# Kernel optimization log

Measured on AMD Instinct MI355X. Metric: run time of the kernel, lower is better.

## Reference

```python
import jax, jax.numpy as jnp
import numpy as np

GRID_SIZE = 5
SPLINE_ORDER = 3
GRID_MIN = -1.0
GRID_MAX = 1.0
H = (GRID_MAX - GRID_MIN) / GRID_SIZE          # grid interval
G0 = GRID_MIN - SPLINE_ORDER * H               # first (extended) knot = grid[:,0]


def _basis_matrix():
    # Uniform B-spline power-basis matrix, same recurrence as the torch code.
    M = np.array([[1.0]], dtype=np.float64)
    scalar = 1.0
    for k in range(2, SPLINE_ORDER + 2):
        t1 = np.pad(M, ((0, 1), (0, 0)))
        t3 = np.pad(M, ((1, 0), (0, 0)))
        t2 = np.zeros((k - 1, k))
        t4 = np.zeros((k - 1, k))
        for i in range(k - 1):
            t2[i, i] = i + 1
            t2[i, i + 1] = k - (i + 2)
            t4[i, i] = -1.0
            t4[i, i + 1] = 1.0
        M = t1 @ t2 + t3 @ t4
        scalar *= 1.0 / (k - 1)
    return (M * scalar).astype(np.float32)

BASIS = jnp.asarray(_basis_matrix())  # (spline_order+1, spline_order+1)


def setup_inputs():
    key = jax.random.key(0)
    k1, k2, k3 = jax.random.split(key, 3)
    N, FIN, FOUT = 2048, 128, 128
    x = jax.random.normal(k1, (N, FIN), dtype=jnp.float32)
    base_weight = jax.random.normal(k2, (FOUT, FIN), dtype=jnp.float32) * 0.1
    spline_weight = jax.random.normal(k3, (FIN, FOUT, GRID_SIZE + SPLINE_ORDER), dtype=jnp.float32) * 0.1
    return {"x": x, "base_weight": base_weight, "spline_weight": spline_weight}


def _forward(x, base_weight, spline_weight):
    N, fin = x.shape
    fout = base_weight.shape[0]
    k = SPLINE_ORDER
    # base branch: SiLU activation then linear
    base_out = jax.nn.silu(x) @ base_weight.T                       # (N, fout)
    # input normalization: Hardtanh around grid center (shift=0, scale=1 for [-1,1])
    shift = (GRID_MIN + GRID_MAX) / 2.0
    scale = (GRID_MAX - GRID_MIN) / 2.0
    xn = jnp.clip((x - shift) / scale, -1.0, 1.0) * scale + shift
    # bucketize: bin index + fractional position (replaces floor/compare + torch.nonzero)
    t = (xn - G0) / H
    fl = jnp.floor(t)
    u1 = t - fl                                                     # (x - interval_floor) / interval
    idx = jnp.clip(fl.astype(jnp.int32), k, k + GRID_SIZE - 1)      # clamped knot-interval index
    cfloor = idx - k                                                # (N, fin) first control point index
    # power bases [1, u, u^2, ..., u^k] -> b-spline basis via basis matrix
    pows = u1[..., None] ** jnp.arange(k + 1, dtype=x.dtype)        # (N, fin, k+1)
    bspl = pows @ BASIS.astype(x.dtype)                             # (N, fin, k+1)
    # faithful to torch: spline_weight.view(out, in, -1) memory reinterpretation
    cp = jnp.reshape(spline_weight, (fout, fin, GRID_SIZE + k))
    gidx = cfloor[..., None] + jnp.arange(k + 1)                    # (N, fin, k+1) control point indices
    i_idx = jnp.arange(fin)[None, :, None]
    gathered = cp[:, i_idx, gidx]                                   # (fout, N, fin, k+1)
    gathered = jnp.transpose(gathered, (1, 0, 2, 3))                # (N, fout, fin, k+1)
    # faithful to torch: .view(N, in, k+1, out) memory reinterpretation
    cpr = jnp.reshape(gathered, (N, fin, k + 1, fout))
    # per-feature spline matmul then sum over in_features (KAN aggregation)
    spline_out = jnp.einsum('nij,nijo->no', bspl, cpr)              # (N, fout)
    return base_out + spline_out


def reference(x, base_weight, spline_weight):
    return _forward(x, base_weight, spline_weight)
```

## Files before the change

kernel.cpp:

```cpp
#include <hip/hip_runtime.h>
#include <hip/hip_bf16.h>
#include <math.h>

typedef __attribute__((ext_vector_type(8))) short short8;
typedef __attribute__((ext_vector_type(4))) float floatx4;
typedef float v4fu __attribute__((ext_vector_type(4), aligned(4)));

#define WS_S    0u
#define WS_P    524288u
#define WS_BT   2621440u
#define WS_C    2916352u
#define WS_T    3178496u

__global__ __launch_bounds__(256) void kan_prep(
    const float* __restrict__ x, const float* __restrict__ bw,
    const float* __restrict__ sw, unsigned char* __restrict__ ws)
{
    __hip_bfloat16* S  = (__hip_bfloat16*)(ws + WS_S);
    __hip_bfloat16* P  = (__hip_bfloat16*)(ws + WS_P);
    __hip_bfloat16* Bt = (__hip_bfloat16*)(ws + WS_BT);
    unsigned char*  cb = ws + WS_C;
    int g = blockIdx.x * 256 + threadIdx.x;
    if (g < 262144) {
        float xv = x[g];
        float si = xv / (1.0f + expf(-xv));
        float xn = fminf(fmaxf(xv, -1.0f), 1.0f);
        float t  = (xn + 2.2f) / 0.4f;
        float u  = t - floorf(t);
        int idx  = (int)floorf(t);
        idx = min(max(idx, 3), 7);
        cb[g] = (unsigned char)(idx - 3);
        float u2 = u*u, u3 = u2*u, om = 1.0f - u;
        float b0 = om*om*om*(1.0f/6.0f);
        float b1 = 0.5f*u3 - u2 + (2.0f/3.0f);
        float b2 = -0.5f*u3 + 0.5f*u2 + 0.5f*u + (1.0f/6.0f);
        float b3 = u3*(1.0f/6.0f);
        S[g] = __float2bfloat16(si);
        P[0*262144 + g] = __float2bfloat16(b0);
        P[1*262144 + g] = __float2bfloat16(b1);
        P[2*262144 + g] = __float2bfloat16(b2);
        P[3*262144 + g] = __float2bfloat16(b3);
    } else if (g < 262144 + 131072) {
        int g2 = g - 262144;
        int a = g2 >> 10, j = g2 & 1023;
        Bt[j*128 + a] = __float2bfloat16(sw[g2]);
    } else if (g < 262144 + 131072 + 16384) {
        int g3 = g - 393216;
        Bt[131072 + g3] = __float2bfloat16(bw[g3]);
    }
}

__global__ __launch_bounds__(256) void kan_gemm(unsigned char* __restrict__ ws)
{
    __shared__ __align__(16) __hip_bfloat16 sA[32 * 128];
    __shared__ __align__(16) __hip_bfloat16 sB[64 * 128];
    const int tid = threadIdx.x;
    const int n0  = blockIdx.x * 32;
    const int j0  = blockIdx.y * 64;
    const __hip_bfloat16* Ap = (const __hip_bfloat16*)(ws + ((j0 >= 1024) ? WS_S : (WS_P + (unsigned)(j0 >> 8) * 524288u)));
    const __hip_bfloat16* Bp = (const __hip_bfloat16*)(ws + WS_BT);

#pragma unroll
    for (int i = 0; i < 2; ++i) {
        int c = tid + 256*i, r = c >> 4, k8 = c & 15;
        *(uint4*)(sA + r*128 + k8*8) = *(const uint4*)(Ap + (n0 + r)*128 + k8*8);
    }
#pragma unroll
    for (int i = 0; i < 4; ++i) {
        int c = tid + 256*i, r = c >> 4, k8 = c & 15;
        *(uint4*)(sB + r*128 + k8*8) = *(const uint4*)(Bp + (j0 + r)*128 + k8*8);
    }
    __syncthreads();

    const int w = tid >> 6, l = tid & 63;
    const int mt = w & 1, nth = w >> 1;
    const int m = l & 15, q = l >> 4;
    floatx4 acc0 = {0.f,0.f,0.f,0.f}, acc1 = {0.f,0.f,0.f,0.f};
    const int arow  = (mt*16      + m)*128 + q*8;
    const int brow0 = (nth*32     + m)*128 + q*8;
    const int brow1 = (nth*32 + 16 + m)*128 + q*8;
#pragma unroll
    for (int kk = 0; kk < 4; ++kk) {
        short8 a  = *(const short8*)(sA + arow  + kk*32);
        short8 b0 = *(const short8*)(sB + brow0 + kk*32);
        short8 b1 = *(const short8*)(sB + brow1 + kk*32);
        acc0 = __builtin_amdgcn_mfma_f32_16x16x32_bf16(a, b0, acc0, 0, 0, 0);
        acc1 = __builtin_amdgcn_mfma_f32_16x16x32_bf16(a, b1, acc1, 0, 0, 0);
    }
    float* T = (float*)(ws + WS_T);
    const int row  = n0 + mt*16 + q*4;
    const int col0 = j0 + nth*32 + m;
#pragma unroll
    for (int r = 0; r < 4; ++r) {
        T[(row + r)*1152 + col0]      = acc0[r];
        T[(row + r)*1152 + col0 + 16] = acc1[r];
    }
}

__global__ __launch_bounds__(256) void kan_epi(const unsigned char* __restrict__ ws,
                                               float* __restrict__ out)
{
    int g = blockIdx.x * 256 + threadIdx.x;
    int n = g >> 5, oh = g & 31;
    const unsigned char* cb = ws + WS_C + n*128;
    const float* Tr = (const float*)(ws + WS_T) + n*1152;
    v4fu acc = *(const v4fu*)(Tr + 1024 + 4*oh);
#pragma unroll
    for (int b = 0; b < 4; ++b) {
        int c = cb[32*b + oh];
        acc += *(const v4fu*)(Tr + 256*b + 8*oh + c);
    }
    *(v4fu*)(out + n*128 + 4*oh) = acc;
}

extern "C" void kernel_launch(void* const* d_in, const int* in_sizes, int n_in,
                              void* d_out, int out_size, void* d_ws, size_t ws_size,
                              hipStream_t stream) {
    const float* x  = (const float*)d_in[0];
    const float* bw = (const float*)d_in[1];
    const float* sw = (const float*)d_in[2];
    float* out = (float*)d_out;
    unsigned char* ws = (unsigned char*)d_ws;
    kan_prep<<<dim3(1600), dim3(256), 0, stream>>>(x, bw, sw, ws);
    kan_gemm<<<dim3(64, 18), dim3(256), 0, stream>>>(ws);
    kan_epi <<<dim3(256), dim3(256), 0, stream>>>(ws, out);
}
```

Measured before the change: 70.70 us.

## Fuse basis computation, GEMM and gather epilogue into one split-K kernel with atomics

Result: slower. 96.22 us (+36.1%).

```diff
diff --git a/kernel.cpp b/kernel.cpp
--- a/kernel.cpp
+++ b/kernel.cpp
@@ -4,113 +4,207 @@
 
 typedef __attribute__((ext_vector_type(8))) short short8;
 typedef __attribute__((ext_vector_type(4))) float floatx4;
-typedef float v4fu __attribute__((ext_vector_type(4), aligned(4)));
-
-#define WS_S    0u
-#define WS_P    524288u
-#define WS_BT   2621440u
-#define WS_C    2916352u
-#define WS_T    3178496u
+
+static __device__ __forceinline__ unsigned short bfbits(float f) {
+    __hip_bfloat16 h = __float2bfloat16(f);
+    unsigned short u;
+    __builtin_memcpy(&u, &h, 2);
+    return u;
+}
+static __device__ __forceinline__ unsigned pack2(float lo, float hi) {
+    return (unsigned)bfbits(lo) | ((unsigned)bfbits(hi) << 16);
+}
 
 __global__ __launch_bounds__(256) void kan_prep(
-    const float* __restrict__ x, const float* __restrict__ bw,
-    const float* __restrict__ sw, unsigned char* __restrict__ ws)
+    const float* __restrict__ bw, const float* __restrict__ sw,
+    unsigned char* __restrict__ ws, float* __restrict__ out)
 {
-    __hip_bfloat16* S  = (__hip_bfloat16*)(ws + WS_S);
-    __hip_bfloat16* P  = (__hip_bfloat16*)(ws + WS_P);
-    __hip_bfloat16* Bt = (__hip_bfloat16*)(ws + WS_BT);
-    unsigned char*  cb = ws + WS_C;
-    int g = blockIdx.x * 256 + threadIdx.x;
-    if (g < 262144) {
-        float xv = x[g];
-        float si = xv / (1.0f + expf(-xv));
-        float xn = fminf(fmaxf(xv, -1.0f), 1.0f);
-        float t  = (xn + 2.2f) / 0.4f;
-        float u  = t - floorf(t);
-        int idx  = (int)floorf(t);
-        idx = min(max(idx, 3), 7);
-        cb[g] = (unsigned char)(idx - 3);
-        float u2 = u*u, u3 = u2*u, om = 1.0f - u;
-        float b0 = om*om*om*(1.0f/6.0f);
-        float b1 = 0.5f*u3 - u2 + (2.0f/3.0f);
-        float b2 = -0.5f*u3 + 0.5f*u2 + 0.5f*u + (1.0f/6.0f);
-        float b3 = u3*(1.0f/6.0f);
-        S[g] = __float2bfloat16(si);
-        P[0*262144 + g] = __float2bfloat16(b0);
-        P[1*262144 + g] = __float2bfloat16(b1);
-        P[2*262144 + g] = __float2bfloat16(b2);
-        P[3*262144 + g] = __float2bfloat16(b3);
-    } else if (g < 262144 + 131072) {
-        int g2 = g - 262144;
-        int a = g2 >> 10, j = g2 & 1023;
-        Bt[j*128 + a] = __float2bfloat16(sw[g2]);
-    } else if (g < 262144 + 131072 + 16384) {
-        int g3 = g - 393216;
-        Bt[131072 + g3] = __float2bfloat16(bw[g3]);
-    }
-}
-
-__global__ __launch_bounds__(256) void kan_gemm(unsigned char* __restrict__ ws)
+    __shared__ float buf[128 * 65];
+    __hip_bfloat16* Bt = (__hip_bfloat16*)ws;
+    const int blk = blockIdx.x;
+    const int tid = threadIdx.x;
+
+    if (blk < 16) {
+        const int a  = tid >> 1;
+        const int jh = (tid & 1) * 32;
+        const float* src = sw + a * 1024 + blk * 64 + jh;
+        float* dst = buf + a * 65 + jh;
+#pragma unroll
+        for (int i = 0; i < 32; ++i) dst[i] = src[i];
+        __syncthreads();
+        const int jl = tid >> 2;
+        const int aq = (tid & 3) * 32;
+        unsigned p[16];
+#pragma unroll
+        for (int i = 0; i < 16; ++i)
+            p[i] = pack2(buf[(aq + 2*i) * 65 + jl], buf[(aq + 2*i + 1) * 65 + jl]);
+        uint4* o = (uint4*)(Bt + (blk * 64 + jl) * 128 + aq);
+        o[0] = make_uint4(p[0], p[1], p[2], p[3]);
+        o[1] = make_uint4(p[4], p[5], p[6], p[7]);
+        o[2] = make_uint4(p[8], p[9], p[10], p[11]);
+        o[3] = make_uint4(p[12], p[13], p[14], p[15]);
+    } else if (blk < 18) {
+        int base = (blk - 16) * 8192 + tid * 32;
+        unsigned p[16];
+#pragma unroll
+        for (int i = 0; i < 8; ++i) {
+            float4 v = *(const float4*)(bw + base + i * 4);
+            p[2*i]     = pack2(v.x, v.y);
+            p[2*i + 1] = pack2(v.z, v.w);
+        }
+        uint4* o = (uint4*)(Bt + 1024 * 128 + base);
+#pragma unroll
+        for (int i = 0; i < 4; ++i)
+            o[i] = make_uint4(p[4*i], p[4*i+1], p[4*i+2], p[4*i+3]);
+    } else {
+        int base = (blk - 18) * 8192 + tid * 32;
+        float4 z = make_float4(0.f, 0.f, 0.f, 0.f);
+#pragma unroll
+        for (int i = 0; i < 8; ++i) *(float4*)(out + base + i * 4) = z;
+    }
+}
+
+#define SB_STR 136
+#define SP_STR 136
+#define ST_STR 68
+#define SC_STR 132
+
+__global__ __launch_bounds__(256) void kan_main(
+    const float* __restrict__ x,
+    const unsigned char* __restrict__ ws,
+    float* __restrict__ out)
 {
-    __shared__ __align__(16) __hip_bfloat16 sA[32 * 128];
-    __shared__ __align__(16) __hip_bfloat16 sB[64 * 128];
+    __shared__ __hip_bfloat16 sP[5 * 16 * SP_STR];
+    __shared__ __hip_bfloat16 sB[64 * SB_STR];
+    __shared__ float sT[16 * ST_STR];
+    __shared__ unsigned char sC[16 * SC_STR];
+
+    const __hip_bfloat16* Bt = (const __hip_bfloat16*)ws;
     const int tid = threadIdx.x;
-    const int n0  = blockIdx.x * 32;
-    const int j0  = blockIdx.y * 64;
-    const __hip_bfloat16* Ap = (const __hip_bfloat16*)(ws + ((j0 >= 1024) ? WS_S : (WS_P + (unsigned)(j0 >> 8) * 524288u)));
-    const __hip_bfloat16* Bp = (const __hip_bfloat16*)(ws + WS_BT);
-
-#pragma unroll
-    for (int i = 0; i < 2; ++i) {
-        int c = tid + 256*i, r = c >> 4, k8 = c & 15;
-        *(uint4*)(sA + r*128 + k8*8) = *(const uint4*)(Ap + (n0 + r)*128 + k8*8);
-    }
-#pragma unroll
-    for (int i = 0; i < 4; ++i) {
-        int c = tid + 256*i, r = c >> 4, k8 = c & 15;
-        *(uint4*)(sB + r*128 + k8*8) = *(const uint4*)(Bp + (j0 + r)*128 + k8*8);
-    }
-    __syncthreads();
+    const int nb  = blockIdx.x >> 2;
+    const int s   = blockIdx.x & 3;
+    const int n0  = nb * 16;
+    const int c_beg = (s == 0) ? 0 : (s == 1) ? 5 : (s == 2) ? 9 : 14;
+    const int c_end = (s == 0) ? 5 : (s == 1) ? 9 : (s == 2) ? 14 : 18;
+
+    {
+        const int r  = tid >> 4;
+        const int i0 = (tid & 15) * 8;
+        float v[8];
+        *(float4*)(v)     = *(const float4*)(x + (n0 + r) * 128 + i0);
+        *(float4*)(v + 4) = *(const float4*)(x + (n0 + r) * 128 + i0 + 4);
+        float A5[5][8];
+        unsigned char cc8[8];
+#pragma unroll
+        for (int i = 0; i < 8; ++i) {
+            float xv = v[i];
+            float si = xv / (1.0f + expf(-xv));
+            float xn = fminf(fmaxf(xv, -1.0f), 1.0f);
+            float t  = (xn + 2.2f) / 0.4f;
+            float u  = t - floorf(t);
+            int idx  = (int)floorf(t);
+            idx = min(max(idx, 3), 7);
+            cc8[i] = (unsigned char)(idx - 3);
+            float u2 = u * u, u3 = u2 * u, om = 1.0f - u;
+            A5[0][i] = om * om * om * (1.0f / 6.0f);
+            A5[1][i] = 0.5f * u3 - u2 + (2.0f / 3.0f);
+            A5[2][i] = -0.5f * u3 + 0.5f * u2 + 0.5f * u + (1.0f / 6.0f);
+            A5[3][i] = u3 * (1.0f / 6.0f);
+            A5[4][i] = si;
+        }
+#pragma unroll
+        for (int g = 0; g < 5; ++g) {
+            unsigned p0 = pack2(A5[g][0], A5[g][1]);
+            unsigned p1 = pack2(A5[g][2], A5[g][3]);
+            unsigned p2 = pack2(A5[g][4], A5[g][5]);
+            unsigned p3 = pack2(A5[g][6], A5[g][7]);
+            *(uint4*)(sP + (g * 16 + r) * SP_STR + i0) = make_uint4(p0, p1, p2, p3);
+        }
+        unsigned u0 = cc8[0] | (cc8[1] << 8) | (cc8[2] << 16) | (cc8[3] << 24);
+        unsigned u1 = cc8[4] | (cc8[5] << 8) | (cc8[6] << 16) | (cc8[7] << 24);
+        *(unsigned*)(sC + r * SC_STR + i0)     = u0;
+        *(unsigned*)(sC + r * SC_STR + i0 + 4) = u1;
+    }
 
     const int w = tid >> 6, l = tid & 63;
-    const int mt = w & 1, nth = w >> 1;
     const int m = l & 15, q = l >> 4;
-    floatx4 acc0 = {0.f,0.f,0.f,0.f}, acc1 = {0.f,0.f,0.f,0.f};
-    const int arow  = (mt*16      + m)*128 + q*8;
-    const int brow0 = (nth*32     + m)*128 + q*8;
-    const int brow1 = (nth*32 + 16 + m)*128 + q*8;
-#pragma unroll
-    for (int kk = 0; kk < 4; ++kk) {
-        short8 a  = *(const short8*)(sA + arow  + kk*32);
-        short8 b0 = *(const short8*)(sB + brow0 + kk*32);
-        short8 b1 = *(const short8*)(sB + brow1 + kk*32);
-        acc0 = __builtin_amdgcn_mfma_f32_16x16x32_bf16(a, b0, acc0, 0, 0, 0);
-        acc1 = __builtin_amdgcn_mfma_f32_16x16x32_bf16(a, b1, acc1, 0, 0, 0);
-    }
-    float* T = (float*)(ws + WS_T);
-    const int row  = n0 + mt*16 + q*4;
-    const int col0 = j0 + nth*32 + m;
-#pragma unroll
-    for (int r = 0; r < 4; ++r) {
-        T[(row + r)*1152 + col0]      = acc0[r];
-        T[(row + r)*1152 + col0 + 16] = acc1[r];
-    }
-}
-
-__global__ __launch_bounds__(256) void kan_epi(const unsigned char* __restrict__ ws,
-                                               float* __restrict__ out)
-{
-    int g = blockIdx.x * 256 + threadIdx.x;
-    int n = g >> 5, oh = g & 31;
-    const unsigned char* cb = ws + WS_C + n*128;
-    const float* Tr = (const float*)(ws + WS_T) + n*1152;
-    v4fu acc = *(const v4fu*)(Tr + 1024 + 4*oh);
-#pragma unroll
-    for (int b = 0; b < 4; ++b) {
-        int c = cb[32*b + oh];
-        acc += *(const v4fu*)(Tr + 256*b + 8*oh + c);
-    }
-    *(v4fu*)(out + n*128 + 4*oh) = acc;
+    const int gn  = tid & 15;
+    const int go8 = tid >> 4;
+    const int br   = tid >> 2;
+    const int bseg = (tid & 3) * 32;
+
+    float racc[8] = {0.f, 0.f, 0.f, 0.f, 0.f, 0.f, 0.f, 0.f};
+
+    uint4 breg[4];
+    {
+        const uint4* src = (const uint4*)(Bt + (c_beg * 64 + br) * 128 + bseg);
+#pragma unroll
+        for (int i = 0; i < 4; ++i) breg[i] = src[i];
+    }
+
+    short8 afrag[4];
+    int cur_g = -1;
+
+    for (int cc = c_beg; cc < c_end; ++cc) {
+#pragma unroll
+        for (int i = 0; i < 4; ++i)
+            *(uint4*)(sB + br * SB_STR + bseg + i * 8) = breg[i];
+        __syncthreads();
+
+        if (cc + 1 < c_end) {
+            const uint4* src = (const uint4*)(Bt + ((cc + 1) * 64 + br) * 128 + bseg);
+#pragma unroll
+            for (int i = 0; i < 4; ++i) breg[i] = src[i];
+        }
+
+        const int g = (cc < 16) ? (cc >> 2) : 4;
+        if (g != cur_g) {
+            cur_g = g;
+#pragma unroll
+            for (int kk = 0; kk < 4; ++kk)
+                afrag[kk] = *(const short8*)(sP + (g * 16 + m) * SP_STR + q * 8 + kk * 32);
+        }
+
+        floatx4 acc = {0.f, 0.f, 0.f, 0.f};
+#pragma unroll
+        for (int kk = 0; kk < 4; ++kk) {
+            short8 bfr = *(const short8*)(sB + (16 * w + m) * SB_STR + q * 8 + kk * 32);
+            acc = __builtin_amdgcn_mfma_f32_16x16x32_bf16(afrag[kk], bfr, acc, 0, 0, 0);
+        }
+#pragma unroll
+        for (int r = 0; r < 4; ++r)
+            sT[(q * 4 + r) * ST_STR + 16 * w + m] = acc[r];
+        __syncthreads();
+
+        const int j0 = cc * 64;
+        if (cc < 16) {
+            const int b    = cc >> 2;
+            const int jrel = j0 & 255;
+            const int ob0  = jrel >> 4;
+            if (go8 >= ob0 && go8 < ob0 + 4) {
+#pragma unroll
+                for (int h = 0; h < 2; ++h) {
+                    int oh  = 2 * go8 + h;
+                    int c   = sC[gn * SC_STR + 32 * b + oh];
+                    int rel = 8 * oh + c - jrel;
+#pragma unroll
+                    for (int ol = 0; ol < 4; ++ol)
+                        racc[4 * h + ol] += sT[gn * ST_STR + rel + ol];
+                }
+            }
+        } else {
+            const int o0 = j0 - 1024;
+            if (go8 >= (o0 >> 3) && go8 < (o0 >> 3) + 8) {
+#pragma unroll
+                for (int i = 0; i < 8; ++i)
+                    racc[i] += sT[gn * ST_STR + 8 * go8 + i - o0];
+            }
+        }
+    }
+
+    float* op = out + (n0 + gn) * 128 + 8 * go8;
+#pragma unroll
+    for (int i = 0; i < 8; ++i) atomicAdd(op + i, racc[i]);
 }
 
 extern "C" void kernel_launch(void* const* d_in, const int* in_sizes, int n_in,
@@ -121,7 +215,6 @@
     const float* sw = (const float*)d_in[2];
     float* out = (float*)d_out;
     unsigned char* ws = (unsigned char*)d_ws;
-    kan_prep<<<dim3(1600), dim3(256), 0, stream>>>(x, bw, sw, ws);
-    kan_gemm<<<dim3(64, 18), dim3(256), 0, stream>>>(ws);
-    kan_epi <<<dim3(256), dim3(256), 0, stream>>>(ws, out);
-}
+    kan_prep<<<dim3(50),  dim3(256), 0, stream>>>(bw, sw, ws, out);
+    kan_main<<<dim3(512), dim3(256), 0, stream>>>(x, ws, out);
+}
```
